# Performance work log

Measured on AMD Instinct MI355X. Metric: run time of the kernel, lower is better.

Reference implementation:

```python
import jax, jax.numpy as jnp
import numpy as np

N_HEAD = 16
DIM = 1024
DIM_HEAD = DIM // N_HEAD
B, S = 4, 2048


def setup_inputs() -> dict:
    key = jax.random.key(0)
    ks = jax.random.split(key, 12)
    p = lambda k, shape: jax.random.normal(k, shape, dtype=jnp.float32) * 0.02
    return {
        "query": jax.random.normal(ks[0], (B, S, DIM), dtype=jnp.float32),
        "key": jax.random.normal(ks[1], (B, S, DIM), dtype=jnp.float32),
        "value": jax.random.normal(ks[2], (B, S, DIM), dtype=jnp.float32),
        "mask": jnp.zeros((B, 1, S, S), dtype=bool),
        "w_q": p(ks[3], (DIM, DIM)), "b_q": jnp.zeros((DIM,), jnp.float32),
        "w_k": p(ks[4], (DIM, DIM)), "b_k": jnp.zeros((DIM,), jnp.float32),
        "w_v": p(ks[5], (DIM, DIM)), "b_v": jnp.zeros((DIM,), jnp.float32),
        "w_o": p(ks[6], (DIM, DIM)), "b_o": jnp.zeros((DIM,), jnp.float32),
    }


def _split_heads(x):
    b, s, _ = x.shape
    return x.reshape(b, s, N_HEAD, DIM_HEAD).transpose(0, 2, 1, 3)  # [b,h,s,dh]


def reference(query, key, value, mask, w_q, b_q, w_k, b_k, w_v, b_v, w_o, b_o):
    # QKV projections (torch Linear: x @ W^T + b)
    Q = _split_heads(query @ w_q.T + b_q)
    K = _split_heads(key @ w_k.T + b_k)
    V = _split_heads(value @ w_v.T + b_v)
    scale = 1.0 / np.sqrt(DIM_HEAD).astype(np.float32)
    scores = jnp.einsum("bhqd,bhkd->bhqk", Q, K) * scale  # [b,h,sq,sk]
    scores = jnp.where(mask, -jnp.inf, scores)
    probs = jax.nn.softmax(scores, axis=-1)
    attn = jnp.einsum("bhqk,bhkd->bhqd", probs, V)
    b, h, s, dh = attn.shape
    merged = attn.transpose(0, 2, 1, 3).reshape(b, s, h * dh)
    return merged @ w_o.T + b_o
```

## Files before the change

kernel.cpp:

```cpp
#include <hip/hip_runtime.h>
#include <hip/hip_bf16.h>
#include <stdint.h>

#define B_N 4
#define S_N 2048
#define DIM_N 1024
#define H_N 16
#define DH_N 64
#define M_ROWS (B_N * S_N)
#define BH_N (B_N * H_N)
#define C1 0.18033688011112042f

typedef unsigned short u16;
typedef __attribute__((ext_vector_type(8))) short short8;
typedef __attribute__((ext_vector_type(4))) float f32x4;
typedef __attribute__((ext_vector_type(16))) float f32x16;

typedef __attribute__((address_space(1))) const void gvoid_t;
typedef __attribute__((address_space(3))) void lvoid_t;

__device__ __forceinline__ u16 f2bf(float f) {
  union { float f; uint32_t u; } c; c.f = f;
  uint32_t u = c.u;
  return (u16)((u + 0x7FFFu + ((u >> 16) & 1u)) >> 16);
}

__device__ __forceinline__ uint32_t pk2(float lo, float hi) {
  float2 f; f.x = lo; f.y = hi;
  __hip_bfloat162 h = __float22bfloat162_rn(f);
  union { __hip_bfloat162 h; uint32_t u; } c; c.h = h;
  return c.u;
}

__global__ void cvt3_kernel(const float* __restrict__ s0, const float* __restrict__ s1,
                            const float* __restrict__ s2, u16* __restrict__ d0,
                            u16* __restrict__ d1, u16* __restrict__ d2_, int n4) {
  const int y = blockIdx.y;
  const float* s = (y == 0) ? s0 : (y == 1 ? s1 : s2);
  u16* d = (y == 0) ? d0 : (y == 1 ? d1 : d2_);
  int i = blockIdx.x * blockDim.x + threadIdx.x;
  if (i >= n4) return;
  float4 v = reinterpret_cast<const float4*>(s)[i];
  ushort4 o;
  o.x = f2bf(v.x); o.y = f2bf(v.y); o.z = f2bf(v.z); o.w = f2bf(v.w);
  reinterpret_cast<ushort4*>(d)[i] = o;
}

__global__ void cvt4_kernel(const float* __restrict__ s0, const float* __restrict__ s1,
                            const float* __restrict__ s2, const float* __restrict__ s3,
                            u16* __restrict__ d0, u16* __restrict__ d1,
                            u16* __restrict__ d2_, u16* __restrict__ d3, int n4) {
  const int y = blockIdx.y;
  const float* s = (y == 0) ? s0 : (y == 1 ? s1 : (y == 2 ? s2 : s3));
  u16* d = (y == 0) ? d0 : (y == 1 ? d1 : (y == 2 ? d2_ : d3));
  int i = blockIdx.x * blockDim.x + threadIdx.x;
  if (i >= n4) return;
  float4 v = reinterpret_cast<const float4*>(s)[i];
  ushort4 o;
  o.x = f2bf(v.x); o.y = f2bf(v.y); o.z = f2bf(v.z); o.w = f2bf(v.w);
  reinterpret_cast<ushort4*>(d)[i] = o;
}

__global__ void pack_mask(const uint8_t* __restrict__ m, uint32_t* __restrict__ bits, int nwords) {
  int i = blockIdx.x * blockDim.x + threadIdx.x;
  if (i >= nwords) return;
  const uint32_t* p = reinterpret_cast<const uint32_t*>(m) + (size_t)i * 8;
  uint32_t out = 0;
#pragma unroll
  for (int w = 0; w < 8; ++w) {
    uint32_t v = p[w];
    if (v & 0x000000FFu) out |= 1u << (w * 4 + 0);
    if (v & 0x0000FF00u) out |= 1u << (w * 4 + 1);
    if (v & 0x00FF0000u) out |= 1u << (w * 4 + 2);
    if (v & 0xFF000000u) out |= 1u << (w * 4 + 3);
  }
  const int b = i >> 17;
  const int rem = i & 131071;
  const int s = rem >> 6, c = rem & 63;
  bits[((size_t)(b * 64 + c) << 11) + s] = out;
}

__global__ __launch_bounds__(256)
void gemm_qkv(const u16* __restrict__ qb, const u16* __restrict__ kb,
              const u16* __restrict__ vb, const u16* __restrict__ wq,
              const u16* __restrict__ wk, const u16* __restrict__ wv,
              const float* __restrict__ bq, const float* __restrict__ bk,
              const float* __restrict__ bv, u16* __restrict__ Qh,
              u16* __restrict__ Kh, u16* __restrict__ Vt)
{
  __shared__ __align__(16) u16 As[128 * 32];
  __shared__ __align__(16) u16 Bs[128 * 32];
  const int z = blockIdx.z;
  const u16* A  = (z == 0) ? qb : (z == 1 ? kb : vb);
  const u16* Bw = (z == 0) ? wq : (z == 1 ? wk : wv);
  const float* bias = (z == 0) ? bq : (z == 1 ? bk : bv);
  u16* outp = (z == 0) ? Qh : (z == 1 ? Kh : Vt);
  const float scale = (z == 0) ? C1 : 1.0f;

  const int m0 = blockIdx.x * 128, n0 = blockIdx.y * 128;
  const int t = threadIdx.x, w = t >> 6;
  const int l = t & 63, lr = l & 15, lg = l >> 4;
  const int wr = (w >> 1) * 64, wc = (w & 1) * 64;
  const int srow = t >> 2;
  const int skoff = (t & 3) * 8;

  f32x4 acc[4][4] = {};

  for (int k0 = 0; k0 < DIM_N; k0 += 32) {
    __syncthreads();
#pragma unroll
    for (int c = 0; c < 2; ++c) {
      const u16* ga = A  + (size_t)(m0 + c * 64 + srow) * DIM_N + k0 + skoff;
      const u16* gb = Bw + (size_t)(n0 + c * 64 + srow) * DIM_N + k0 + skoff;
      u16* la = &As[(c * 64 + 16 * w) * 32];
      u16* lb = &Bs[(c * 64 + 16 * w) * 32];
      __builtin_amdgcn_global_load_lds((gvoid_t*)ga, (lvoid_t*)la, 16, 0, 0);
      __builtin_amdgcn_global_load_lds((gvoid_t*)gb, (lvoid_t*)lb, 16, 0, 0);
    }
    __syncthreads();

    short8 af[4], bfr[4];
#pragma unroll
    for (int mf = 0; mf < 4; ++mf)
      af[mf] = *reinterpret_cast<const short8*>(&As[(wr + mf * 16 + lr) * 32 + lg * 8]);
#pragma unroll
    for (int nf = 0; nf < 4; ++nf)
      bfr[nf] = *reinterpret_cast<const short8*>(&Bs[(wc + nf * 16 + lr) * 32 + lg * 8]);
#pragma unroll
    for (int mf = 0; mf < 4; ++mf)
#pragma unroll
      for (int nf = 0; nf < 4; ++nf)
        acc[mf][nf] = __builtin_amdgcn_mfma_f32_16x16x32_bf16(af[mf], bfr[nf], acc[mf][nf], 0, 0, 0);
  }

  float bv4[4];
#pragma unroll
  for (int nf = 0; nf < 4; ++nf) bv4[nf] = bias[n0 + wc + nf * 16 + lr];

#pragma unroll
  for (int mf = 0; mf < 4; ++mf)
#pragma unroll
    for (int nf = 0; nf < 4; ++nf)
#pragma unroll
      for (int r = 0; r < 4; ++r) {
        int grow = m0 + wr + mf * 16 + lg * 4 + r;
        int gcol = n0 + wc + nf * 16 + lr;
        float v = (acc[mf][nf][r] + bv4[nf]) * scale;
        int b = grow >> 11, s = grow & 2047;
        int h = gcol >> 6, d = gcol & 63;
        size_t idx;
        if (z < 2) {
          idx = ((size_t)(b * H_N + h) * S_N + s) * DH_N + d;
        } else {
          int sp = ((((s & 15) + 4) & 8) ? (s ^ 12) : s);
          idx = ((size_t)(b * H_N + h) * DH_N + d) * S_N + sp;
        }
        outp[idx] = f2bf(v);
      }
}

__global__ __launch_bounds__(256)
void gemm_out(const u16* __restrict__ A, const u16* __restrict__ Bw,
              const float* __restrict__ bias, float* __restrict__ outp)
{
  __shared__ __align__(16) u16 As[128 * 32];
  __shared__ __align__(16) u16 Bs[128 * 32];
  const int m0 = blockIdx.x * 128, n0 = blockIdx.y * 128;
  const int t = threadIdx.x, w = t >> 6;
  const int l = t & 63, lr = l & 15, lg = l >> 4;
  const int wr = (w >> 1) * 64, wc = (w & 1) * 64;
  const int srow = t >> 2;
  const int skoff = (t & 3) * 8;

  f32x4 acc[4][4] = {};

  for (int k0 = 0; k0 < DIM_N; k0 += 32) {
    __syncthreads();
#pragma unroll
    for (int c = 0; c < 2; ++c) {
      const u16* ga = A  + (size_t)(m0 + c * 64 + srow) * DIM_N + k0 + skoff;
      const u16* gb = Bw + (size_t)(n0 + c * 64 + srow) * DIM_N + k0 + skoff;
      u16* la = &As[(c * 64 + 16 * w) * 32];
      u16* lb = &Bs[(c * 64 + 16 * w) * 32];
      __builtin_amdgcn_global_load_lds((gvoid_t*)ga, (lvoid_t*)la, 16, 0, 0);
      __builtin_amdgcn_global_load_lds((gvoid_t*)gb, (lvoid_t*)lb, 16, 0, 0);
    }
    __syncthreads();

    short8 af[4], bfr[4];
#pragma unroll
    for (int mf = 0; mf < 4; ++mf)
      af[mf] = *reinterpret_cast<const short8*>(&As[(wr + mf * 16 + lr) * 32 + lg * 8]);
#pragma unroll
    for (int nf = 0; nf < 4; ++nf)
      bfr[nf] = *reinterpret_cast<const short8*>(&Bs[(wc + nf * 16 + lr) * 32 + lg * 8]);
#pragma unroll
    for (int mf = 0; mf < 4; ++mf)
#pragma unroll
      for (int nf = 0; nf < 4; ++nf)
        acc[mf][nf] = __builtin_amdgcn_mfma_f32_16x16x32_bf16(af[mf], bfr[nf], acc[mf][nf], 0, 0, 0);
  }

  float bv4[4];
#pragma unroll
  for (int nf = 0; nf < 4; ++nf) bv4[nf] = bias[n0 + wc + nf * 16 + lr];

#pragma unroll
  for (int mf = 0; mf < 4; ++mf)
#pragma unroll
    for (int nf = 0; nf < 4; ++nf)
#pragma unroll
      for (int r = 0; r < 4; ++r) {
        int grow = m0 + wr + mf * 16 + lg * 4 + r;
        int gcol = n0 + wc + nf * 16 + lr;
        outp[(size_t)grow * DIM_N + gcol] = acc[mf][nf][r] + bv4[nf];
      }
}

#define AT_WAVES 4
#define QPW 64
#define KVB 64
#define NCH (S_N / KVB)

__global__ __launch_bounds__(256, 2)
void attn_kernel(const u16* __restrict__ Qh, const u16* __restrict__ Kh,
                 const u16* __restrict__ Vt, const uint32_t* __restrict__ mbits,
                 u16* __restrict__ AO)
{
  __shared__ __align__(16) u16 K_lds[2][KVB * DH_N];
  __shared__ __align__(16) u16 V_lds[2][DH_N * KVB];

  const int t = threadIdx.x;
  const int w = t >> 6, l = t & 63;
  const int l31 = l & 31, hl = l >> 5;
  const int kx = l31 & 7;

  const int bx = blockIdx.x;
  const int bh = (bx & 7) * 8 + (bx >> 3);
  const int b = bh >> 4, h = bh & 15;
  const int q0 = blockIdx.y * (AT_WAVES * QPW) + w * QPW;

  const u16* Qp = Qh + (size_t)bh * S_N * DH_N;
  const u16* Kp = Kh + (size_t)bh * S_N * DH_N;
  const u16* Vp = Vt + (size_t)bh * DH_N * S_N;
  const uint32_t* mq0 = mbits + ((size_t)b << 17) + q0 + l31;
  const uint32_t* mq1 = mq0 + 32;

  short8 qf0[4], qf1[4];
#pragma unroll
  for (int u = 0; u < 4; ++u) {
    qf0[u] = *reinterpret_cast<const short8*>(
        Qp + (size_t)(q0 + l31) * DH_N + u * 16 + hl * 8);
    qf1[u] = *reinterpret_cast<const short8*>(
        Qp + (size_t)(q0 + 32 + l31) * DH_N + u * 16 + hl * 8);
  }

  f32x16 o00 = {}, o01 = {}, o10 = {}, o11 = {};
  float lr0 = 0.f, lr1 = 0.f;

  auto STAGE = [&](int buf, int kc) {
#pragma unroll
    for (int p = 0; p < 2; ++p) {
      const int s = p * 256 + t;
      const int row = s >> 3, up = s & 7, j = up ^ (row & 7);
      const u16* gk = Kp + (size_t)(kc * KVB + row) * DH_N + j * 8;
      const u16* gv = Vp + (size_t)row * S_N + kc * KVB + j * 8;
      u16* lk = &K_lds[buf][(p * 256 + w * 64) * 8];
      u16* lv = &V_lds[buf][(p * 256 + w * 64) * 8];
      __builtin_amdgcn_global_load_lds((gvoid_t*)gk, (lvoid_t*)lk, 16, 0, 0);
      __builtin_amdgcn_global_load_lds((gvoid_t*)gv, (lvoid_t*)lv, 16, 0, 0);
    }
  };

  auto softpv = [&](f32x16& z, uint32_t mw, float& lr,
                    f32x16& oA, f32x16& oB, const short8 vf[2][2]) {
    if (mw) {
#pragma unroll
      for (int r = 0; r < 16; ++r)
        if ((mw >> ((r & 3) + 8 * (r >> 2) + 4 * hl)) & 1) z[r] = -1e30f;
    }

    float p[16];
#pragma unroll
    for (int r = 0; r < 16; ++r) p[r] = __builtin_amdgcn_exp2f(z[r]);
    float a8[8], a4[4];
#pragma unroll
    for (int r = 0; r < 8; ++r) a8[r] = p[2 * r] + p[2 * r + 1];
#pragma unroll
    for (int r = 0; r < 4; ++r) a4[r] = a8[2 * r] + a8[2 * r + 1];
    lr += (a4[0] + a4[1]) + (a4[2] + a4[3]);

    union { uint32_t u[4]; short8 s8; } pf0, pf1;
    pf0.u[0] = pk2(p[0], p[1]);   pf0.u[1] = pk2(p[2], p[3]);
    pf0.u[2] = pk2(p[4], p[5]);   pf0.u[3] = pk2(p[6], p[7]);
    pf1.u[0] = pk2(p[8], p[9]);   pf1.u[1] = pk2(p[10], p[11]);
    pf1.u[2] = pk2(p[12], p[13]); pf1.u[3] = pk2(p[14], p[15]);

    __builtin_amdgcn_s_setprio(1);
    oA = __builtin_amdgcn_mfma_f32_32x32x16_bf16(vf[0][0], pf0.s8, oA, 0, 0, 0);
    oB = __builtin_amdgcn_mfma_f32_32x32x16_bf16(vf[0][1], pf0.s8, oB, 0, 0, 0);
    oA = __builtin_amdgcn_mfma_f32_32x32x16_bf16(vf[1][0], pf1.s8, oA, 0, 0, 0);
    oB = __builtin_amdgcn_mfma_f32_32x32x16_bf16(vf[1][1], pf1.s8, oB, 0, 0, 0);
    __builtin_amdgcn_s_setprio(0);
  };

  auto half = [&](int buf, int hh, uint32_t mwg0, uint32_t mwg1) {
    const int kb = hh * 32;
    short8 kf[4];
#pragma unroll
    for (int u = 0; u < 4; ++u)
      kf[u] = *reinterpret_cast<const short8*>(
          &K_lds[buf][(kb + l31) * DH_N + (((2 * u + hl) ^ kx) * 8)]);

    f32x16 z0 = {}, z1 = {};
    __builtin_amdgcn_s_setprio(1);
    z0 = __builtin_amdgcn_mfma_f32_32x32x16_bf16(kf[0], qf0[0], z0, 0, 0, 0);
    z1 = __builtin_amdgcn_mfma_f32_32x32x16_bf16(kf[0], qf1[0], z1, 0, 0, 0);
    z0 = __builtin_amdgcn_mfma_f32_32x32x16_bf16(kf[1], qf0[1], z0, 0, 0, 0);
    z1 = __builtin_amdgcn_mfma_f32_32x32x16_bf16(kf[1], qf1[1], z1, 0, 0, 0);
    z0 = __builtin_amdgcn_mfma_f32_32x32x16_bf16(kf[2], qf0[2], z0, 0, 0, 0);
    z1 = __builtin_amdgcn_mfma_f32_32x32x16_bf16(kf[2], qf1[2], z1, 0, 0, 0);
    z0 = __builtin_amdgcn_mfma_f32_32x32x16_bf16(kf[3], qf0[3], z0, 0, 0, 0);
    z1 = __builtin_amdgcn_mfma_f32_32x32x16_bf16(kf[3], qf1[3], z1, 0, 0, 0);
    __builtin_amdgcn_s_setprio(0);

    short8 vf[2][2];
#pragma unroll
    for (int ks = 0; ks < 2; ++ks)
#pragma unroll
      for (int nf = 0; nf < 2; ++nf)
        vf[ks][nf] = *reinterpret_cast<const short8*>(
            &V_lds[buf][(nf * 32 + l31) * KVB + (((hh * 4 + ks * 2 + hl) ^ kx) * 8)]);

    softpv(z0, mwg0, lr0, o00, o01, vf);
    softpv(z1, mwg1, lr1, o10, o11, vf);
  };

  STAGE(0, 0);
  __syncthreads();
  int cb = 0;
  for (int kc = 0; kc < NCH; ++kc) {
    uint32_t mw00 = mq0[(size_t)(2 * kc) * S_N];
    uint32_t mw10 = mq1[(size_t)(2 * kc) * S_N];
    uint32_t mw01 = mq0[(size_t)(2 * kc + 1) * S_N];
    uint32_t mw11 = mq1[(size_t)(2 * kc + 1) * S_N];
    if (kc + 1 < NCH) STAGE(cb ^ 1, kc + 1);
    half(cb, 0, mw00, mw10);
    half(cb, 1, mw01, mw11);
    __syncthreads();
    cb ^= 1;
  }

  auto fin = [&](float lr, int qg, const f32x16& oA, const f32x16& oB) {
    float l_tot = lr + __shfl_xor(lr, 32);
    float inv_l = 1.0f / l_tot;
    u16* orow = AO + ((size_t)b * S_N + q0 + qg + l31) * DIM_N + h * DH_N;
#pragma unroll
    for (int gg = 0; gg < 4; ++gg) {
      ushort4 v4;
      v4.x = f2bf(oA[gg * 4 + 0] * inv_l);
      v4.y = f2bf(oA[gg * 4 + 1] * inv_l);
      v4.z = f2bf(oA[gg * 4 + 2] * inv_l);
      v4.w = f2bf(oA[gg * 4 + 3] * inv_l);
      *reinterpret_cast<ushort4*>(orow + gg * 8 + hl * 4) = v4;
      ushort4 w4;
      w4.x = f2bf(oB[gg * 4 + 0] * inv_l);
      w4.y = f2bf(oB[gg * 4 + 1] * inv_l);
      w4.z = f2bf(oB[gg * 4 + 2] * inv_l);
      w4.w = f2bf(oB[gg * 4 + 3] * inv_l);
      *reinterpret_cast<ushort4*>(orow + 32 + gg * 8 + hl * 4) = w4;
    }
  };
  fin(lr0, 0, o00, o01);
  fin(lr1, 32, o10, o11);
}

extern "C" void kernel_launch(void* const* d_in, const int* in_sizes, int n_in,
                              void* d_out, int out_size, void* d_ws, size_t ws_size,
                              hipStream_t stream)
{
  const float*   q_in = (const float*)d_in[0];
  const float*   k_in = (const float*)d_in[1];
  const float*   v_in = (const float*)d_in[2];
  const uint8_t* mask = (const uint8_t*)d_in[3];
  const float*   w_q  = (const float*)d_in[4];
  const float*   b_q  = (const float*)d_in[5];
  const float*   w_k  = (const float*)d_in[6];
  const float*   b_k  = (const float*)d_in[7];
  const float*   w_v  = (const float*)d_in[8];
  const float*   b_v  = (const float*)d_in[9];
  const float*   w_o  = (const float*)d_in[10];
  const float*   b_o  = (const float*)d_in[11];

  char* ws = (char*)d_ws;
  size_t off = 0;
  auto alloc = [&](size_t bytes) -> char* {
    char* p = ws + off;
    off += (bytes + 255) & ~(size_t)255;
    return p;
  };
  const size_t act_b = (size_t)M_ROWS * DIM_N * 2;
  const size_t w_b   = (size_t)DIM_N * DIM_N * 2;
  const int    nmw   = B_N * S_N * (S_N / 32);
  u16* qb  = (u16*)alloc(act_b);
  u16* kb  = (u16*)alloc(act_b);
  u16* vb  = (u16*)alloc(act_b);
  u16* wqb = (u16*)alloc(w_b);
  u16* wkb = (u16*)alloc(w_b);
  u16* wvb = (u16*)alloc(w_b);
  u16* wob = (u16*)alloc(w_b);
  u16* Qh  = (u16*)alloc(act_b);
  u16* Kh  = (u16*)alloc(act_b);
  u16* Vt  = (u16*)alloc(act_b);
  uint32_t* mbits = (uint32_t*)alloc((size_t)nmw * 4);
  u16* AO  = qb;

  const int n4a = M_ROWS * DIM_N / 4;
  const int n4w = DIM_N * DIM_N / 4;
  cvt3_kernel<<<dim3(n4a / 256, 3), 256, 0, stream>>>(q_in, k_in, v_in, qb, kb, vb, n4a);
  cvt4_kernel<<<dim3(n4w / 256, 4), 256, 0, stream>>>(w_q, w_k, w_v, w_o,
                                                      wqb, wkb, wvb, wob, n4w);
  pack_mask<<<nmw / 256, 256, 0, stream>>>(mask, mbits, nmw);

  gemm_qkv<<<dim3(M_ROWS / 128, DIM_N / 128, 3), 256, 0, stream>>>(
      qb, kb, vb, wqb, wkb, wvb, b_q, b_k, b_v, Qh, Kh, Vt);

  attn_kernel<<<dim3(64, 8), 256, 0, stream>>>(Qh, Kh, Vt, mbits, AO);

  gemm_out<<<dim3(M_ROWS / 128, DIM_N / 128), 256, 0, stream>>>(
      AO, wob, b_o, (float*)d_out);
}
```

Measured before the change: 230.1 us.

## Merge prep kernels, compute softmax row sums via MFMA, relax attention launch bounds

The three conversion and mask-packing kernels become a single prep kernel that dispatches on block index, removing two launches. In attention, the per-lane scalar reduction of exp values is replaced by an extra MFMA against a constant ones vector, which accumulates row sums in matrix registers and drops the final cross-lane shuffle. The attention launch bounds go from two blocks per CU to one, which allows more registers per thread at possible cost to occupancy. The extra MFMAs add matrix-unit work and two more 16-float accumulators per wave.

```diff
diff --git a/kernel.cpp b/kernel.cpp
--- a/kernel.cpp
+++ b/kernel.cpp
@@ -32,52 +32,56 @@
   return c.u;
 }
 
-__global__ void cvt3_kernel(const float* __restrict__ s0, const float* __restrict__ s1,
-                            const float* __restrict__ s2, u16* __restrict__ d0,
-                            u16* __restrict__ d1, u16* __restrict__ d2_, int n4) {
-  const int y = blockIdx.y;
-  const float* s = (y == 0) ? s0 : (y == 1 ? s1 : s2);
-  u16* d = (y == 0) ? d0 : (y == 1 ? d1 : d2_);
-  int i = blockIdx.x * blockDim.x + threadIdx.x;
-  if (i >= n4) return;
-  float4 v = reinterpret_cast<const float4*>(s)[i];
-  ushort4 o;
-  o.x = f2bf(v.x); o.y = f2bf(v.y); o.z = f2bf(v.z); o.w = f2bf(v.w);
-  reinterpret_cast<ushort4*>(d)[i] = o;
-}
-
-__global__ void cvt4_kernel(const float* __restrict__ s0, const float* __restrict__ s1,
-                            const float* __restrict__ s2, const float* __restrict__ s3,
-                            u16* __restrict__ d0, u16* __restrict__ d1,
-                            u16* __restrict__ d2_, u16* __restrict__ d3, int n4) {
-  const int y = blockIdx.y;
-  const float* s = (y == 0) ? s0 : (y == 1 ? s1 : (y == 2 ? s2 : s3));
-  u16* d = (y == 0) ? d0 : (y == 1 ? d1 : (y == 2 ? d2_ : d3));
-  int i = blockIdx.x * blockDim.x + threadIdx.x;
-  if (i >= n4) return;
-  float4 v = reinterpret_cast<const float4*>(s)[i];
-  ushort4 o;
-  o.x = f2bf(v.x); o.y = f2bf(v.y); o.z = f2bf(v.z); o.w = f2bf(v.w);
-  reinterpret_cast<ushort4*>(d)[i] = o;
-}
-
-__global__ void pack_mask(const uint8_t* __restrict__ m, uint32_t* __restrict__ bits, int nwords) {
-  int i = blockIdx.x * blockDim.x + threadIdx.x;
-  if (i >= nwords) return;
-  const uint32_t* p = reinterpret_cast<const uint32_t*>(m) + (size_t)i * 8;
-  uint32_t out = 0;
-#pragma unroll
-  for (int w = 0; w < 8; ++w) {
-    uint32_t v = p[w];
-    if (v & 0x000000FFu) out |= 1u << (w * 4 + 0);
-    if (v & 0x0000FF00u) out |= 1u << (w * 4 + 1);
-    if (v & 0x00FF0000u) out |= 1u << (w * 4 + 2);
-    if (v & 0xFF000000u) out |= 1u << (w * 4 + 3);
-  }
-  const int b = i >> 17;
-  const int rem = i & 131071;
-  const int s = rem >> 6, c = rem & 63;
-  bits[((size_t)(b * 64 + c) << 11) + s] = out;
+#define CVT3_BLKS (3 * 8192)
+#define CVT4_BLKS (4 * 1024)
+#define PACK_BLKS 2048
+
+__global__ __launch_bounds__(256)
+void prep_kernel(const float* __restrict__ q_in, const float* __restrict__ k_in,
+                 const float* __restrict__ v_in, const float* __restrict__ w_q,
+                 const float* __restrict__ w_k, const float* __restrict__ w_v,
+                 const float* __restrict__ w_o, const uint8_t* __restrict__ m,
+                 u16* __restrict__ qb, u16* __restrict__ kb, u16* __restrict__ vb,
+                 u16* __restrict__ wqb, u16* __restrict__ wkb, u16* __restrict__ wvb,
+                 u16* __restrict__ wob, uint32_t* __restrict__ bits)
+{
+  const int bid = blockIdx.x;
+  if (bid < CVT3_BLKS) {
+    const int y = bid >> 13;
+    const int i = ((bid & 8191) << 8) + threadIdx.x;
+    const float* s = (y == 0) ? q_in : (y == 1 ? k_in : v_in);
+    u16* d = (y == 0) ? qb : (y == 1 ? kb : vb);
+    float4 v = reinterpret_cast<const float4*>(s)[i];
+    ushort4 o;
+    o.x = f2bf(v.x); o.y = f2bf(v.y); o.z = f2bf(v.z); o.w = f2bf(v.w);
+    reinterpret_cast<ushort4*>(d)[i] = o;
+  } else if (bid < CVT3_BLKS + CVT4_BLKS) {
+    const int r = bid - CVT3_BLKS;
+    const int y = r >> 10;
+    const int i = ((r & 1023) << 8) + threadIdx.x;
+    const float* s = (y == 0) ? w_q : (y == 1 ? w_k : (y == 2 ? w_v : w_o));
+    u16* d = (y == 0) ? wqb : (y == 1 ? wkb : (y == 2 ? wvb : wob));
+    float4 v = reinterpret_cast<const float4*>(s)[i];
+    ushort4 o;
+    o.x = f2bf(v.x); o.y = f2bf(v.y); o.z = f2bf(v.z); o.w = f2bf(v.w);
+    reinterpret_cast<ushort4*>(d)[i] = o;
+  } else {
+    const int i = ((bid - CVT3_BLKS - CVT4_BLKS) << 8) + threadIdx.x;
+    const uint32_t* p = reinterpret_cast<const uint32_t*>(m) + (size_t)i * 8;
+    uint32_t out = 0;
+#pragma unroll
+    for (int w = 0; w < 8; ++w) {
+      uint32_t v = p[w];
+      if (v & 0x000000FFu) out |= 1u << (w * 4 + 0);
+      if (v & 0x0000FF00u) out |= 1u << (w * 4 + 1);
+      if (v & 0x00FF0000u) out |= 1u << (w * 4 + 2);
+      if (v & 0xFF000000u) out |= 1u << (w * 4 + 3);
+    }
+    const int b = i >> 17;
+    const int rem = i & 131071;
+    const int s = rem >> 6, c = rem & 63;
+    bits[((size_t)(b * 64 + c) << 11) + s] = out;
+  }
 }
 
 __global__ __launch_bounds__(256)
@@ -222,7 +226,7 @@
 #define KVB 64
 #define NCH (S_N / KVB)
 
-__global__ __launch_bounds__(256, 2)
+__global__ __launch_bounds__(256, 1)
 void attn_kernel(const u16* __restrict__ Qh, const u16* __restrict__ Kh,
                  const u16* __restrict__ Vt, const uint32_t* __restrict__ mbits,
                  u16* __restrict__ AO)
@@ -246,6 +250,13 @@
   const uint32_t* mq0 = mbits + ((size_t)b << 17) + q0 + l31;
   const uint32_t* mq1 = mq0 + 32;
 
+  short8 ones8;
+  {
+    const short ov = (l31 == 0 || l31 == 4) ? (short)0x3F80 : (short)0;
+#pragma unroll
+    for (int j = 0; j < 8; ++j) ones8[j] = ov;
+  }
+
   short8 qf0[4], qf1[4];
 #pragma unroll
   for (int u = 0; u < 4; ++u) {
@@ -256,7 +267,7 @@
   }
 
   f32x16 o00 = {}, o01 = {}, o10 = {}, o11 = {};
-  float lr0 = 0.f, lr1 = 0.f;
+  f32x16 lacc0 = {}, lacc1 = {};
 
   auto STAGE = [&](int buf, int kc) {
 #pragma unroll
@@ -272,7 +283,7 @@
     }
   };
 
-  auto softpv = [&](f32x16& z, uint32_t mw, float& lr,
+  auto softpv = [&](f32x16& z, uint32_t mw, f32x16& lacc,
                     f32x16& oA, f32x16& oB, const short8 vf[2][2]) {
     if (mw) {
 #pragma unroll
@@ -283,12 +294,6 @@
     float p[16];
 #pragma unroll
     for (int r = 0; r < 16; ++r) p[r] = __builtin_amdgcn_exp2f(z[r]);
-    float a8[8], a4[4];
-#pragma unroll
-    for (int r = 0; r < 8; ++r) a8[r] = p[2 * r] + p[2 * r + 1];
-#pragma unroll
-    for (int r = 0; r < 4; ++r) a4[r] = a8[2 * r] + a8[2 * r + 1];
-    lr += (a4[0] + a4[1]) + (a4[2] + a4[3]);
 
     union { uint32_t u[4]; short8 s8; } pf0, pf1;
     pf0.u[0] = pk2(p[0], p[1]);   pf0.u[1] = pk2(p[2], p[3]);
@@ -299,8 +304,10 @@
     __builtin_amdgcn_s_setprio(1);
     oA = __builtin_amdgcn_mfma_f32_32x32x16_bf16(vf[0][0], pf0.s8, oA, 0, 0, 0);
     oB = __builtin_amdgcn_mfma_f32_32x32x16_bf16(vf[0][1], pf0.s8, oB, 0, 0, 0);
+    lacc = __builtin_amdgcn_mfma_f32_32x32x16_bf16(ones8, pf0.s8, lacc, 0, 0, 0);
     oA = __builtin_amdgcn_mfma_f32_32x32x16_bf16(vf[1][0], pf1.s8, oA, 0, 0, 0);
     oB = __builtin_amdgcn_mfma_f32_32x32x16_bf16(vf[1][1], pf1.s8, oB, 0, 0, 0);
+    lacc = __builtin_amdgcn_mfma_f32_32x32x16_bf16(ones8, pf1.s8, lacc, 0, 0, 0);
     __builtin_amdgcn_s_setprio(0);
   };
 
@@ -332,8 +339,8 @@
         vf[ks][nf] = *reinterpret_cast<const short8*>(
             &V_lds[buf][(nf * 32 + l31) * KVB + (((hh * 4 + ks * 2 + hl) ^ kx) * 8)]);
 
-    softpv(z0, mwg0, lr0, o00, o01, vf);
-    softpv(z1, mwg1, lr1, o10, o11, vf);
+    softpv(z0, mwg0, lacc0, o00, o01, vf);
+    softpv(z1, mwg1, lacc1, o10, o11, vf);
   };
 
   STAGE(0, 0);
@@ -351,8 +358,7 @@
     cb ^= 1;
   }
 
-  auto fin = [&](float lr, int qg, const f32x16& oA, const f32x16& oB) {
-    float l_tot = lr + __shfl_xor(lr, 32);
+  auto fin = [&](float l_tot, int qg, const f32x16& oA, const f32x16& oB) {
     float inv_l = 1.0f / l_tot;
     u16* orow = AO + ((size_t)b * S_N + q0 + qg + l31) * DIM_N + h * DH_N;
 #pragma unroll
@@ -371,8 +377,8 @@
       *reinterpret_cast<ushort4*>(orow + 32 + gg * 8 + hl * 4) = w4;
     }
   };
-  fin(lr0, 0, o00, o01);
-  fin(lr1, 32, o10, o11);
+  fin(lacc0[0], 0, o00, o01);
+  fin(lacc1[0], 32, o10, o11);
 }
 
 extern "C" void kernel_launch(void* const* d_in, const int* in_sizes, int n_in,
@@ -415,12 +421,9 @@
   uint32_t* mbits = (uint32_t*)alloc((size_t)nmw * 4);
   u16* AO  = qb;
 
-  const int n4a = M_ROWS * DIM_N / 4;
-  const int n4w = DIM_N * DIM_N / 4;
-  cvt3_kernel<<<dim3(n4a / 256, 3), 256, 0, stream>>>(q_in, k_in, v_in, qb, kb, vb, n4a);
-  cvt4_kernel<<<dim3(n4w / 256, 4), 256, 0, stream>>>(w_q, w_k, w_v, w_o,
-                                                      wqb, wkb, wvb, wob, n4w);
-  pack_mask<<<nmw / 256, 256, 0, stream>>>(mask, mbits, nmw);
+  prep_kernel<<<CVT3_BLKS + CVT4_BLKS + PACK_BLKS, 256, 0, stream>>>(
+      q_in, k_in, v_in, w_q, w_k, w_v, w_o, mask,
+      qb, kb, vb, wqb, wkb, wvb, wob, mbits);
 
   gemm_qkv<<<dim3(M_ROWS / 128, DIM_N / 128, 3), 256, 0, stream>>>(
       qb, kb, vb, wqb, wkb, wvb, b_q, b_k, b_v, Qh, Kh, Vt);
```

New measurement: 278.1 us. +20.9%, slower.
